# Optimization experiments

Hardware: AMD Instinct MI355X
Metric: run time of the kernel (lower is better)

## Reference

```python
import jax, jax.numpy as jnp
import numpy as np

B, LQ, LKV = 2, 4096, 2048
DQ = DK = DV = 1024
H, DQK, DHV = 16, 64, 64
DOUT = 1024


def _band_mask(span, stride):
    # additive mask: 0 where 0 <= row - col*stride < span, else -inf
    rows = jnp.arange(LQ)[:, None]
    cols = jnp.arange(LKV)[None, :]
    s = rows - cols * stride
    valid = (s >= 0) & (s < span)
    return jnp.where(valid, 0.0, -jnp.inf).astype(jnp.float32)  # [LQ, LKV]


def setup_inputs() -> dict:
    key = jax.random.key(0)
    ks = jax.random.split(key, 7)
    return {
        "q": jax.random.normal(ks[0], (B, LQ, DQ), jnp.float32),
        "k": jax.random.normal(ks[1], (B, LKV, DK), jnp.float32),
        "v": jax.random.normal(ks[2], (B, LKV, DV), jnp.float32),
        # Linear weights stored as [in, out] (x @ W == torch Linear with W.T)
        "Wq": jax.random.normal(ks[3], (DQ, H * DQK), jnp.float32) / np.sqrt(DQ).astype(np.float32),
        "Wk": jax.random.normal(ks[4], (DK, H * DQK), jnp.float32) / np.sqrt(DK).astype(np.float32),
        "Wv": jax.random.normal(ks[5], (DV, H * DHV), jnp.float32) / np.sqrt(DV).astype(np.float32),
        "Wo": jax.random.normal(ks[6], (H * DHV, DOUT), jnp.float32) / np.sqrt(H * DHV).astype(np.float32),
        "span": 16,
        "stride": 2,
    }


def reference(q, k, v, Wq, Wk, Wv, Wo, span, stride):
    mask = _band_mask(span, stride)  # [LQ, LKV]
    Q = (q @ Wq).reshape(B, LQ, H, DQK)   # [B, LQ, H, DQK]
    K = (k @ Wk).reshape(B, LKV, H, DQK)  # [B, LKV, H, DQK]
    V = (v @ Wv).reshape(B, LKV, H, DHV)  # [B, LKV, H, DHV]
    scores = jnp.einsum("bqhd,bkhd->bhqk", Q, K) + mask  # [B, H, LQ, LKV]
    # NOTE: original code softmaxes over dim 2 == the QUERY axis (faithful)
    attn = jax.nn.softmax(scores, axis=2)
    ctx = jnp.einsum("bhqk,bkhd->bqhd", attn, V).reshape(B, LQ, H * DHV)
    return ctx @ Wo  # [B, LQ, DOUT]
```

## Files before the change

### kernel.cpp

```cpp
#include <hip/hip_runtime.h>
#include <cstdint>
#include <cstddef>


typedef _Float16 f16;
typedef _Float16 f16x4 __attribute__((ext_vector_type(4)));
typedef _Float16 f16x8 __attribute__((ext_vector_type(8)));
typedef float v4f __attribute__((ext_vector_type(4)));

#define B_  2
#define LQ_ 4096
#define LKV_ 2048
#define DMODEL 1024
#define NH 16
#define HD 64
#define SPAN 16
#define STRIDE 2

#define NQ_ELEMS  ((size_t)B_ * LQ_ * DMODEL)
#define NKV_ELEMS ((size_t)B_ * LKV_ * DMODEL)

__device__ __forceinline__ void async_copy16(const f16* g, f16* l) {
    __builtin_amdgcn_global_load_lds((const __attribute__((address_space(1))) void*)g,
                                     (__attribute__((address_space(3))) void*)l, 16, 0, 0);
}

__global__ __launch_bounds__(256)
void prep_all(const float* __restrict__ q, const float* __restrict__ k,
              const float* __restrict__ v, f16* __restrict__ qh,
              f16* __restrict__ kh, f16* __restrict__ vh,
              const float* __restrict__ W0, const float* __restrict__ W1,
              const float* __restrict__ W2, const float* __restrict__ W3,
              f16* __restrict__ T0, f16* __restrict__ T1,
              f16* __restrict__ T2, f16* __restrict__ T3) {
    const int t = threadIdx.x;
    if (blockIdx.x < 16384) {
        size_t i = ((size_t)blockIdx.x * 256 + t) * 4;
        const float* src;
        f16* dst;
        if (i < NQ_ELEMS) {
            src = q + i; dst = qh + i;
        } else if (i < NQ_ELEMS + NKV_ELEMS) {
            src = k + (i - NQ_ELEMS); dst = kh + (i - NQ_ELEMS);
        } else {
            src = v + (i - NQ_ELEMS - NKV_ELEMS); dst = vh + (i - NQ_ELEMS - NKV_ELEMS);
        }
        float4 x = *(const float4*)src;
        f16x4 o = {(f16)x.x, (f16)x.y, (f16)x.z, (f16)x.w};
        *(f16x4*)dst = o;
    } else {
        const int bid = blockIdx.x - 16384;
        const int z = bid >> 8, rem = bid & 255;
        const int bx = rem & 15, byy = rem >> 4;
        const float* W;
        f16* Wt;
        switch (z) {
            case 0: W = W0; Wt = T0; break;
            case 1: W = W1; Wt = T1; break;
            case 2: W = W2; Wt = T2; break;
            default: W = W3; Wt = T3; break;
        }
        __shared__ float tile[64][65];
        const int r0 = byy * 64, c0 = bx * 64;
        const int tx = t & 63, ty = t >> 6;
        for (int i = ty; i < 64; i += 4)
            tile[i][tx] = W[(long)(r0 + i) * DMODEL + c0 + tx];
        __syncthreads();
        for (int i = ty; i < 64; i += 4)
            Wt[(long)(c0 + i) * DMODEL + r0 + tx] = (f16)tile[tx][i];
    }
}

template <bool OUT_F32>
__device__ __forceinline__ void gemm_body(const f16* __restrict__ A,
                                          const f16* __restrict__ Bt,
                                          void* __restrict__ Cv,
                                          int rowTile, int colTile) {
    constexpr int K = DMODEL, N = DMODEL;
    __shared__ f16 As[128 * 32];
    __shared__ f16 Bs[128 * 32];
    const int t = threadIdx.x;
    const int lane = t & 63;
    const int w = t >> 6;
    const int wm = w >> 1, wn = w & 1;
    const long rowBase = (long)rowTile * 128;
    const long colBase = (long)colTile * 128;
    const int qrow = lane & 15;
    const int quad = lane >> 4;

    v4f acc[4][4] = {};

    const int srow = w * 32 + (lane >> 2);
    const int scol = (lane & 3) * 8;
    const f16* aptr = A + (rowBase + srow) * (long)K + scol;
    const f16* bptr = Bt + (colBase + srow) * (long)K + scol;
    f16* lA0 = &As[srow * 32 + scol];
    f16* lA1 = &As[(srow + 16) * 32 + scol];
    f16* lB0 = &Bs[srow * 32 + scol];
    f16* lB1 = &Bs[(srow + 16) * 32 + scol];

    for (int k0 = 0; k0 < K; k0 += 32) {
        async_copy16(aptr + k0, lA0);
        async_copy16(aptr + 16 * (long)K + k0, lA1);
        async_copy16(bptr + k0, lB0);
        async_copy16(bptr + 16 * (long)K + k0, lB1);
        __syncthreads();
        f16x8 af[4], bf[4];
#pragma unroll
        for (int mt = 0; mt < 4; ++mt)
            af[mt] = *(const f16x8*)(&As[(wm * 64 + mt * 16 + qrow) * 32 + quad * 8]);
#pragma unroll
        for (int nt = 0; nt < 4; ++nt)
            bf[nt] = *(const f16x8*)(&Bs[(wn * 64 + nt * 16 + qrow) * 32 + quad * 8]);
#pragma unroll
        for (int mt = 0; mt < 4; ++mt)
#pragma unroll
            for (int nt = 0; nt < 4; ++nt)
                acc[mt][nt] = __builtin_amdgcn_mfma_f32_16x16x32_f16(af[mt], bf[nt],
                                                                     acc[mt][nt], 0, 0, 0);
        __syncthreads();
    }

#pragma unroll
    for (int mt = 0; mt < 4; ++mt)
#pragma unroll
        for (int nt = 0; nt < 4; ++nt) {
            const long col = colBase + wn * 64 + nt * 16 + qrow;
#pragma unroll
            for (int r = 0; r < 4; ++r) {
                const long row = rowBase + wm * 64 + mt * 16 + quad * 4 + r;
                if (OUT_F32)
                    ((float*)Cv)[row * (long)N + col] = acc[mt][nt][r];
                else
                    ((f16*)Cv)[row * (long)N + col] = (f16)acc[mt][nt][r];
            }
        }
}

__global__ __launch_bounds__(256, 2)
void gemm_qkv(const f16* __restrict__ A0, const f16* __restrict__ A1,
              const f16* __restrict__ A2, const f16* __restrict__ B0,
              const f16* __restrict__ B1, const f16* __restrict__ B2,
              f16* __restrict__ C0, f16* __restrict__ C1, f16* __restrict__ C2) {
    const int id = blockIdx.x;
    const int xcd = id & 7;
    const int g = id >> 3;
    const int ct = g & 7;
    int rowIdx = (g >> 3) + xcd * 16;
    const f16 *A, *Bt;
    f16* C;
    if (rowIdx < 64) {
        A = A0; Bt = B0; C = C0;
    } else if (rowIdx < 96) {
        A = A1; Bt = B1; C = C1; rowIdx -= 64;
    } else {
        A = A2; Bt = B2; C = C2; rowIdx -= 96;
    }
    gemm_body<false>(A, Bt, (void*)C, rowIdx, ct);
}

__global__ __launch_bounds__(256, 2)
void gemm_out(const f16* __restrict__ A, const f16* __restrict__ Bt,
              float* __restrict__ C) {
    const int id = blockIdx.x;
    const int xcd = id & 7;
    const int g = id >> 3;
    const int ct = g & 7;
    const int rowIdx = (g >> 3) + xcd * 8;
    gemm_body<true>(A, Bt, (void*)C, rowIdx, ct);
}

__global__ __launch_bounds__(256)
void attn_scores(const f16* __restrict__ Q, const f16* __restrict__ Km,
                 float* __restrict__ attnw) {
    const int c0 = blockIdx.x * 4, b = blockIdx.y;
    const int t = threadIdx.x;
    __shared__ f16 Qs[24 * 1032];
    __shared__ f16 Ks[4 * 1032];

#pragma unroll
    for (int it = 0; it < 12; ++it) {
        const int ch = t + 256 * it;
        const int row = ch >> 7, off = (ch & 127) * 8;
        int qq = 2 * c0 + row;
        if (qq > LQ_ - 1) qq = LQ_ - 1;
        f16x8 x = *(const f16x8*)(Q + (size_t)(b * LQ_ + qq) * DMODEL + off);
        const int h = off >> 6, bb = (off >> 3) & 7;
        *(f16x8*)(&Qs[row * 1032 + h * 64 + ((bb + h) & 7) * 8]) = x;
    }
#pragma unroll
    for (int it = 0; it < 2; ++it) {
        const int ch = t + 256 * it;
        const int row = ch >> 7, off = (ch & 127) * 8;
        f16x8 x = *(const f16x8*)(Km + (size_t)(b * LKV_ + c0 + row) * DMODEL + off);
        const int h = off >> 6, bb = (off >> 3) & 7;
        *(f16x8*)(&Ks[row * 1032 + h * 64 + ((bb + h) & 7) * 8]) = x;
    }
    __syncthreads();

    const int h = t >> 4, j = t & 15;
#pragma unroll
    for (int ci = 0; ci < 4; ++ci) {
        const int c = c0 + ci;
        const int q = STRIDE * c + j;
        const int row = 2 * ci + j;
        float a = 0.f;
#pragma unroll
        for (int bb = 0; bb < 8; ++bb) {
            const int off = h * 64 + ((bb + h) & 7) * 8;
            f16x8 qv = *(const f16x8*)(&Qs[row * 1032 + off]);
            f16x8 kv = *(const f16x8*)(&Ks[ci * 1032 + off]);
#pragma unroll
            for (int u = 0; u < 8; ++u) a += (float)qv[u] * (float)kv[u];
        }
        float s = (q < LQ_) ? a : -1e30f;
        float m = s;
#pragma unroll
        for (int o = 1; o < 16; o <<= 1) m = fmaxf(m, __shfl_xor(m, o, 64));
        float p = (q < LQ_) ? __expf(s - m) : 0.f;
        float sum = p;
#pragma unroll
        for (int o = 1; o < 16; o <<= 1) sum += __shfl_xor(sum, o, 64);
        attnw[(size_t)((b * LKV_ + c) * NH + h) * SPAN + j] = p / sum;
    }
}

__global__ __launch_bounds__(256)
void ctx_gather(const float* __restrict__ attnw, const f16* __restrict__ V,
                f16* __restrict__ ctx) {
    const int q0 = blockIdx.x * 16, b = blockIdx.y;
    const int t = threadIdx.x;
    const int kbase = (q0 >> 1) - 7;
    __shared__ f16 Vs[16 * 1024];
    __shared__ float A_lds[16 * 256];

#pragma unroll
    for (int it = 0; it < 8; ++it) {
        const int ch = t + 256 * it;
        const int row = ch >> 7, off = (ch & 127) * 8;
        int k = kbase + row;
        k = (k < 0) ? 0 : ((k > LKV_ - 1) ? LKV_ - 1 : k);
        *(f16x8*)(&Vs[row * 1024 + off]) =
            *(const f16x8*)(V + (size_t)(b * LKV_ + k) * DMODEL + off);
    }
#pragma unroll
    for (int it = 0; it < 4; ++it) {
        const int ch = t + 256 * it;
        const int row = ch >> 6, off = (ch & 63) * 4;
        int k = kbase + row;
        k = (k < 0) ? 0 : ((k > LKV_ - 1) ? LKV_ - 1 : k);
        *(float4*)(&A_lds[row * 256 + off]) =
            *(const float4*)(attnw + (size_t)(b * LKV_ + k) * 256 + off);
    }
    __syncthreads();

    const int d = t & 63;
    const int hg = t >> 6;
#pragma unroll
    for (int ql = 0; ql < 16; ++ql) {
        const int q = q0 + ql;
        const int j0 = q & 1;
        float acc[4] = {0.f, 0.f, 0.f, 0.f};
#pragma unroll
        for (int i = 0; i < SPAN / STRIDE; ++i) {
            const int kq = (q >> 1) - i;
            if (kq < 0) break;
            const int rr = kq - kbase;
#pragma unroll
            for (int hh = 0; hh < 4; ++hh) {
                const int h = hg * 4 + hh;
                acc[hh] += A_lds[rr * 256 + h * 16 + j0 + 2 * i] *
                           (float)Vs[rr * 1024 + h * 64 + d];
            }
        }
        f16* crow = ctx + (size_t)(b * LQ_ + q) * DMODEL;
#pragma unroll
        for (int hh = 0; hh < 4; ++hh) {
            const int h = hg * 4 + hh;
            crow[h * HD + d] = (f16)acc[hh];
        }
    }
}

extern "C" void kernel_launch(void* const* d_in, const int* in_sizes, int n_in,
                              void* d_out, int out_size, void* d_ws, size_t ws_size,
                              hipStream_t stream) {
    const float* q  = (const float*)d_in[0];
    const float* k  = (const float*)d_in[1];
    const float* v  = (const float*)d_in[2];
    const float* Wq = (const float*)d_in[3];
    const float* Wk = (const float*)d_in[4];
    const float* Wv = (const float*)d_in[5];
    const float* Wo = (const float*)d_in[6];
    float* out = (float*)d_out;

    const size_t NW = (size_t)DMODEL * DMODEL;

    char* p = (char*)d_ws;
    f16* qh  = (f16*)p; p += NQ_ELEMS * 2;
    f16* kh  = (f16*)p; p += NKV_ELEMS * 2;
    f16* vh  = (f16*)p; p += NKV_ELEMS * 2;
    f16* WqT = (f16*)p; p += NW * 2;
    f16* WkT = (f16*)p; p += NW * 2;
    f16* WvT = (f16*)p; p += NW * 2;
    f16* WoT = (f16*)p; p += NW * 2;
    f16* Qh  = (f16*)p; p += NQ_ELEMS * 2;
    f16* Kh  = (f16*)p; p += NKV_ELEMS * 2;
    f16* Vh  = (f16*)p; p += NKV_ELEMS * 2;
    float* attnw = (float*)p; p += (size_t)B_ * LKV_ * NH * SPAN * 4;
    f16* ctxh = (f16*)p; p += NQ_ELEMS * 2;

    prep_all<<<dim3(17408), 256, 0, stream>>>(q, k, v, qh, kh, vh,
                                              Wq, Wk, Wv, Wo, WqT, WkT, WvT, WoT);

    gemm_qkv<<<dim3(1024), 256, 0, stream>>>(qh, kh, vh, WqT, WkT, WvT, Qh, Kh, Vh);

    attn_scores<<<dim3(LKV_ / 4, B_), 256, 0, stream>>>(Qh, Kh, attnw);

    ctx_gather<<<dim3(LQ_ / 16, B_), 256, 0, stream>>>(attnw, Vh, ctxh);

    gemm_out<<<dim3(512), 256, 0, stream>>>(ctxh, WoT, out);
}
```

Before: 241.7 us.

## Double GEMM K-tile to 64 with XOR-swizzled LDS layout

The projection GEMM now stages 64-wide K slices of A and B into LDS per iteration instead of 32, which halves the number of barrier pairs per tile. The LDS layout applies an XOR swizzle on 16-byte chunks, keyed by row, so the fragment reads for the MFMA avoid bank conflicts. This costs twice the shared memory per block, which may lower occupancy, and there is still no double buffering, so loads and compute remain serialized.

```diff
diff --git a/kernel.cpp b/kernel.cpp
--- a/kernel.cpp
+++ b/kernel.cpp
@@ -77,8 +77,8 @@
                                           void* __restrict__ Cv,
                                           int rowTile, int colTile) {
     constexpr int K = DMODEL, N = DMODEL;
-    __shared__ f16 As[128 * 32];
-    __shared__ f16 Bs[128 * 32];
+    __shared__ f16 As[128 * 64];
+    __shared__ f16 Bs[128 * 64];
     const int t = threadIdx.x;
     const int lane = t & 63;
     const int w = t >> 6;
@@ -90,34 +90,38 @@
 
     v4f acc[4][4] = {};
 
-    const int srow = w * 32 + (lane >> 2);
-    const int scol = (lane & 3) * 8;
-    const f16* aptr = A + (rowBase + srow) * (long)K + scol;
-    const f16* bptr = Bt + (colBase + srow) * (long)K + scol;
-    f16* lA0 = &As[srow * 32 + scol];
-    f16* lA1 = &As[(srow + 16) * 32 + scol];
-    f16* lB0 = &Bs[srow * 32 + scol];
-    f16* lB1 = &Bs[(srow + 16) * 32 + scol];
-
-    for (int k0 = 0; k0 < K; k0 += 32) {
-        async_copy16(aptr + k0, lA0);
-        async_copy16(aptr + 16 * (long)K + k0, lA1);
-        async_copy16(bptr + k0, lB0);
-        async_copy16(bptr + 16 * (long)K + k0, lB1);
+    const int srow = t >> 3;
+    const int schunk = t & 7;
+    const int gchunk = schunk ^ (srow & 7);
+    const f16* aptr = A + (rowBase + srow) * (long)K + gchunk * 8;
+    const f16* bptr = Bt + (colBase + srow) * (long)K + gchunk * 8;
+    f16* lA = &As[srow * 64 + schunk * 8];
+    f16* lB = &Bs[srow * 64 + schunk * 8];
+
+    for (int k0 = 0; k0 < K; k0 += 64) {
+#pragma unroll
+        for (int i = 0; i < 4; ++i) {
+            async_copy16(aptr + k0 + i * 32 * (long)K, lA + i * 2048);
+            async_copy16(bptr + k0 + i * 32 * (long)K, lB + i * 2048);
+        }
         __syncthreads();
-        f16x8 af[4], bf[4];
-#pragma unroll
-        for (int mt = 0; mt < 4; ++mt)
-            af[mt] = *(const f16x8*)(&As[(wm * 64 + mt * 16 + qrow) * 32 + quad * 8]);
-#pragma unroll
-        for (int nt = 0; nt < 4; ++nt)
-            bf[nt] = *(const f16x8*)(&Bs[(wn * 64 + nt * 16 + qrow) * 32 + quad * 8]);
-#pragma unroll
-        for (int mt = 0; mt < 4; ++mt)
+#pragma unroll
+        for (int s = 0; s < 2; ++s) {
+            const int xk = (s * 4 + quad) ^ (qrow & 7);
+            f16x8 af[4], bf[4];
+#pragma unroll
+            for (int mt = 0; mt < 4; ++mt)
+                af[mt] = *(const f16x8*)(&As[(wm * 64 + mt * 16 + qrow) * 64 + xk * 8]);
 #pragma unroll
             for (int nt = 0; nt < 4; ++nt)
-                acc[mt][nt] = __builtin_amdgcn_mfma_f32_16x16x32_f16(af[mt], bf[nt],
-                                                                     acc[mt][nt], 0, 0, 0);
+                bf[nt] = *(const f16x8*)(&Bs[(wn * 64 + nt * 16 + qrow) * 64 + xk * 8]);
+#pragma unroll
+            for (int mt = 0; mt < 4; ++mt)
+#pragma unroll
+                for (int nt = 0; nt < 4; ++nt)
+                    acc[mt][nt] = __builtin_amdgcn_mfma_f32_16x16x32_f16(
+                        af[mt], bf[nt], acc[mt][nt], 0, 0, 0);
+        }
         __syncthreads();
     }
 
```

After: 229.3 us. 5.1% less time.
